# Optimization experiments

Hardware: AMD Instinct MI355X
Metric: run time of the kernel (lower is better)

## Reference

```python
import jax, jax.numpy as jnp
import numpy as np

B, C, H, W = 4, 64, 64, 64
CI = C // 4  # inter_channels for q/k convs and SE fc


def setup_inputs() -> dict:
    key = jax.random.key(0)
    ks = jax.random.split(key, 12)
    s = lambda k, shape, fan: jax.random.normal(k, shape, jnp.float32) * (1.0 / np.sqrt(fan))
    return {
        "ftr": jax.random.normal(ks[0], (B, C, H, W), jnp.float32),
        "wq": s(ks[1], (CI, C), C), "bq": jnp.zeros((CI,), jnp.float32),
        "wk": s(ks[2], (CI, C), C), "bk": jnp.zeros((CI,), jnp.float32),
        "wv": s(ks[3], (C, C), C),  "bv": jnp.zeros((C,), jnp.float32),
        "delta": jnp.array([0.1], jnp.float32),
        "w_avg1": s(ks[4], (CI, C), C), "w_avg2": s(ks[5], (C, CI), CI),
        "w_max1": s(ks[6], (CI, C), C), "w_max2": s(ks[7], (C, CI), CI),
    }


def reference(ftr, wq, bq, wk, bk, wv, bv, delta, w_avg1, w_avg2, w_max1, w_max2):
    b, c, h, w = ftr.shape
    p = h * w
    x = ftr.reshape(b, c, p)                                   # [B,C,P]
    q = jnp.einsum('oc,bcp->bpo', wq, x) + bq                  # [B,P,CI]
    k = jnp.einsum('oc,bcp->bop', wk, x) + bk[:, None]         # [B,CI,P]
    v = jnp.einsum('oc,bcp->bop', wv, x) + bv[:, None]         # [B,C,P]
    scores = jnp.einsum('bpo,boq->bpq', q, k)                  # [B,P,P]
    weights = jax.nn.softmax(scores, axis=1)                   # softmax over dim=1 (queries), as in torch code
    G = jnp.einsum('bcp,bpq->bcq', v, weights).reshape(b, c, h, w)
    out = delta[0] * G + ftr
    # ChannelRecalibration (SE with avg+max pooling)
    f_avg = jnp.mean(out, axis=(2, 3))                         # [B,C]
    f_max = jnp.max(out, axis=(2, 3))                          # [B,C]
    a = jax.nn.relu(f_avg @ w_avg1.T) @ w_avg2.T
    m = jax.nn.relu(f_max @ w_max1.T) @ w_max2.T
    gate = jax.nn.sigmoid(a + m)[:, :, None, None]
    return gate * out
```

## Files before the change

### kernel.cpp

```cpp
#include <hip/hip_runtime.h>
#include <math.h>

#define PP 4096

typedef __attribute__((ext_vector_type(8))) short short8;
typedef __attribute__((ext_vector_type(4))) float float4v;

__device__ __forceinline__ short f2bf(float f) {
    union { float f; unsigned u; } v; v.f = f;
    unsigned r = v.u + 0x7FFFu + ((v.u >> 16) & 1u);
    return (short)(r >> 16);
}

__global__ __launch_bounds__(256) void qkv_kernel(
    const float* __restrict__ ftr, const float* __restrict__ wq, const float* __restrict__ bq,
    const float* __restrict__ wk, const float* __restrict__ bk,
    const float* __restrict__ wv, const float* __restrict__ bv,
    short* __restrict__ q16, short* __restrict__ k16, short* __restrict__ v_sw)
{
    __shared__ float xs[64][68] __attribute__((aligned(16)));
    __shared__ float wvs[64][68] __attribute__((aligned(16)));
    __shared__ float wq_t[64][20] __attribute__((aligned(16)));
    __shared__ float wk_t[64][20] __attribute__((aligned(16)));

    const int b  = blockIdx.x >> 6;
    const int p0 = (blockIdx.x & 63) << 6;
    const int tid = threadIdx.x;

    for (int idx = tid; idx < 1024; idx += 256) {
        int c = idx >> 4, j4 = (idx & 15) << 2;
        *(float4*)&xs[c][j4] = *(const float4*)(ftr + ((size_t)(b * 64 + c)) * PP + p0 + j4);
    }
    for (int idx = tid; idx < 1024; idx += 256) {
        int r = idx >> 4, j4 = (idx & 15) << 2;
        *(float4*)&wvs[r][j4] = *(const float4*)(wv + r * 64 + j4);
    }
    for (int idx = tid; idx < 1024; idx += 256) {
        int o = idx >> 6, c2 = idx & 63;
        wq_t[c2][o] = wq[idx];
        wk_t[c2][o] = wk[idx];
    }
    __syncthreads();

    {
        const int wg = tid >> 6, qd = (tid >> 4) & 3, cc = tid & 15;
        const int c = wg * 16 + cc;
        const int ktg0 = p0 >> 5;
        const float bvc = bv[c];
        #pragma unroll
        for (int kt = 0; kt < 2; ++kt) {
            const int col = kt * 32 + qd * 8;
            float a[8] = {0.f,0.f,0.f,0.f,0.f,0.f,0.f,0.f};
            #pragma unroll 8
            for (int c2 = 0; c2 < 64; ++c2) {
                float w = wvs[c][c2];
                float4 xa = *(const float4*)&xs[c2][col];
                float4 xb = *(const float4*)&xs[c2][col + 4];
                a[0] += w * xa.x; a[1] += w * xa.y; a[2] += w * xa.z; a[3] += w * xa.w;
                a[4] += w * xb.x; a[5] += w * xb.y; a[6] += w * xb.z; a[7] += w * xb.w;
            }
            short8 pv;
            #pragma unroll
            for (int jj = 0; jj < 8; ++jj) pv[jj] = f2bf(a[jj] + bvc);
            *(short8*)(v_sw + ((size_t)(b * 128 + ktg0 + kt)) * 2048 + tid * 8) = pv;
        }
    }

    {
        const int p_l = tid >> 2, sel = tid & 3;
        const int half = sel & 1, arr = sel >> 1;
        const float* Wtr = arr ? &wk_t[0][0] : &wq_t[0][0];
        float a[8] = {0.f,0.f,0.f,0.f,0.f,0.f,0.f,0.f};
        #pragma unroll 8
        for (int c2 = 0; c2 < 64; ++c2) {
            float x = xs[c2][p_l];
            float4 wA = *(const float4*)(Wtr + c2 * 20 + half * 8);
            float4 wB = *(const float4*)(Wtr + c2 * 20 + half * 8 + 4);
            a[0] += wA.x * x; a[1] += wA.y * x; a[2] += wA.z * x; a[3] += wA.w * x;
            a[4] += wB.x * x; a[5] += wB.y * x; a[6] += wB.z * x; a[7] += wB.w * x;
        }
        const float* bias = arr ? bk : bq;
        const float scl = arr ? 1.0f : 1.4426950408889634f;
        short8 pq;
        #pragma unroll
        for (int oo = 0; oo < 8; ++oo)
            pq[oo] = f2bf((a[oo] + bias[half * 8 + oo]) * scl);
        short* dst = (arr ? k16 : q16) + (((size_t)(b * PP + p0 + p_l)) << 4) + half * 8;
        *(short8*)dst = pq;
    }
}

__global__ __launch_bounds__(256, 2) void attn_kernel(
    const short* __restrict__ q16, const short* __restrict__ k16,
    const short* __restrict__ v_sw,
    const float* __restrict__ ftr, const float* __restrict__ delta,
    float* __restrict__ out, float* __restrict__ psum, float* __restrict__ pmax)
{
    __shared__ char smem[34304] __attribute__((aligned(16)));
    short* Wt   = (short*)smem;
    float* Obuf = (float*)smem;
    float* lb   = (float*)(smem + 33792);

    const int b    = blockIdx.x >> 7;
    const int qblk = blockIdx.x & 127;
    const int q0   = qblk << 5;
    const int tid  = threadIdx.x;
    const int lane = tid & 63;
    const int n    = lane & 15;
    const int quad = lane >> 4;
    const int ph   = tid >> 6;

    const short8 z8 = {0,0,0,0,0,0,0,0};
    const float4v zf4 = {0.f,0.f,0.f,0.f};

    short8 bkf[2];
    #pragma unroll
    for (int mt = 0; mt < 2; ++mt) {
        bkf[mt] = z8;
        if (quad < 2)
            bkf[mt] = *(const short8*)(k16 + ((size_t)(b * PP + q0 + mt * 16 + n) << 4) + quad * 8);
    }

    const short* vbase = v_sw + (size_t)b * 262144 + lane * 8;
    const short* qbase = q16 + ((size_t)(b * PP + n) << 4) + (quad & 1) * 8;
    short* wbase = Wt + ph * 2048;

    float4v acc[2][4];
    #pragma unroll
    for (int mt = 0; mt < 2; ++mt)
        #pragma unroll
        for (int nt = 0; nt < 4; ++nt) acc[mt][nt] = zf4;
    float lsum[2] = {0.f, 0.f};

    const int pt0 = ph * 1024;
    short8 aq[2][4];
    #pragma unroll
    for (int f = 0; f < 4; ++f) { aq[0][f] = z8; aq[1][f] = z8; }
    if (quad < 2) {
        #pragma unroll
        for (int f = 0; f < 4; ++f)
            aq[0][f] = *(const short8*)(qbase + (size_t)(pt0 + f * 16) * 16);
    }

    #pragma unroll 2
    for (int it = 0; it < 16; ++it) {
        const int cb = it & 1;
        const int pt = pt0 + it * 64;
        const int ktg0 = pt >> 5;

        short8 vf[2][4];
        #pragma unroll
        for (int kt = 0; kt < 2; ++kt)
            #pragma unroll
            for (int nt = 0; nt < 4; ++nt)
                vf[kt][nt] = *(const short8*)(vbase + (size_t)((ktg0 + kt) * 4 + nt) * 512);

        if (it < 15 && quad < 2) {
            const short* qb = qbase + (size_t)(pt + 64) * 16;
            #pragma unroll
            for (int f = 0; f < 4; ++f)
                aq[cb ^ 1][f] = *(const short8*)(qb + f * 256);
        }

        float4v sf[4][2];
        #pragma unroll
        for (int f = 0; f < 4; ++f)
            #pragma unroll
            for (int mt = 0; mt < 2; ++mt)
                sf[f][mt] = __builtin_amdgcn_mfma_f32_16x16x32_bf16(aq[cb][f], bkf[mt], zf4, 0, 0, 0);

        #pragma unroll
        for (int mt = 0; mt < 2; ++mt) {
            short* wrow = wbase + (mt * 16 + n) * 64;
            #pragma unroll
            for (int f = 0; f < 4; ++f) {
                float w0 = __builtin_amdgcn_exp2f(sf[f][mt][0]);
                float w1 = __builtin_amdgcn_exp2f(sf[f][mt][1]);
                float w2 = __builtin_amdgcn_exp2f(sf[f][mt][2]);
                float w3 = __builtin_amdgcn_exp2f(sf[f][mt][3]);
                lsum[mt] += (w0 + w1) + (w2 + w3);
                uint2 pk;
                pk.x = __builtin_amdgcn_perm(__float_as_uint(w1), __float_as_uint(w0), 0x07060302u);
                pk.y = __builtin_amdgcn_perm(__float_as_uint(w3), __float_as_uint(w2), 0x07060302u);
                const int g = (f * 4 + quad) ^ ((n & 7) << 1);
                *(uint2*)(wrow + g * 4) = pk;
            }
        }

        short8 wa[2][2];
        #pragma unroll
        for (int mt = 0; mt < 2; ++mt) {
            const short* rrow = wbase + (mt * 16 + n) * 64;
            #pragma unroll
            for (int kt = 0; kt < 2; ++kt) {
                const int gr = (kt * 8 + quad * 2) ^ ((n & 7) << 1);
                wa[mt][kt] = *(const short8*)(rrow + gr * 4);
            }
        }
        #pragma unroll
        for (int mt = 0; mt < 2; ++mt)
            #pragma unroll
            for (int kt = 0; kt < 2; ++kt)
                #pragma unroll
                for (int nt = 0; nt < 4; ++nt)
                    acc[mt][nt] = __builtin_amdgcn_mfma_f32_16x16x32_bf16(wa[mt][kt], vf[kt][nt], acc[mt][nt], 0, 0, 0);
    }

    lsum[0] += __shfl_xor(lsum[0], 16); lsum[0] += __shfl_xor(lsum[0], 32);
    lsum[1] += __shfl_xor(lsum[1], 16); lsum[1] += __shfl_xor(lsum[1], 32);
    if (quad == 0) {
        lb[ph * 32 + n]      = lsum[0];
        lb[ph * 32 + 16 + n] = lsum[1];
    }
    __syncthreads();
    #pragma unroll
    for (int mt = 0; mt < 2; ++mt)
        #pragma unroll
        for (int nt = 0; nt < 4; ++nt)
            #pragma unroll
            for (int r = 0; r < 4; ++r)
                Obuf[ph * 2112 + (mt * 16 + quad * 4 + r) * 66 + nt * 16 + n] = acc[mt][nt][r];
    __syncthreads();

    const int c = tid >> 2, qq = tid & 3;
    const float dlt = delta[0];
    const size_t gbase = ((size_t)(b * 64 + c)) * PP + q0 + qq * 8;
    float4 f0 = *(const float4*)(ftr + gbase);
    float4 f1 = *(const float4*)(ftr + gbase + 4);
    float fr[8] = {f0.x, f0.y, f0.z, f0.w, f1.x, f1.y, f1.z, f1.w};
    float ov[8];
    float s8 = 0.f, m8 = -3.4e38f;
    #pragma unroll
    for (int i = 0; i < 8; ++i) {
        const int q = qq * 8 + i;
        float o = Obuf[q * 66 + c] + Obuf[2112 + q * 66 + c]
                + Obuf[4224 + q * 66 + c] + Obuf[6336 + q * 66 + c];
        float lq = lb[q] + lb[32 + q] + lb[64 + q] + lb[96 + q];
        float v = dlt * o / lq + fr[i];
        ov[i] = v; s8 += v; m8 = fmaxf(m8, v);
    }
    float4 o0 = {ov[0], ov[1], ov[2], ov[3]};
    float4 o1 = {ov[4], ov[5], ov[6], ov[7]};
    *(float4*)(out + gbase)     = o0;
    *(float4*)(out + gbase + 4) = o1;

    s8 += __shfl_xor(s8, 1); s8 += __shfl_xor(s8, 2);
    m8 = fmaxf(m8, __shfl_xor(m8, 1)); m8 = fmaxf(m8, __shfl_xor(m8, 2));
    if (qq == 0) {
        psum[((size_t)b * 128 + qblk) * 64 + c] = s8;
        pmax[((size_t)b * 128 + qblk) * 64 + c] = m8;
    }
}

__global__ __launch_bounds__(256) void reduce_gate_kernel(
    const float* __restrict__ psum, const float* __restrict__ pmax,
    const float* __restrict__ w_avg1, const float* __restrict__ w_avg2,
    const float* __restrict__ w_max1, const float* __restrict__ w_max2,
    float* __restrict__ gate)
{
    const int b = blockIdx.x, t = threadIdx.x;
    const int c = t & 63, ch = t >> 6;
    float s = 0.f, m = -3.4e38f;
    for (int i = 0; i < 32; ++i) {
        const int part = ch * 32 + i;
        s += psum[((size_t)b * 128 + part) * 64 + c];
        m = fmaxf(m, pmax[((size_t)b * 128 + part) * 64 + c]);
    }
    __shared__ float ss[4][64], sm[4][64], fa[64], fm[64], ha[16], hm[16];
    ss[ch][c] = s; sm[ch][c] = m;
    __syncthreads();
    if (t < 64) {
        fa[t] = (ss[0][t] + ss[1][t] + ss[2][t] + ss[3][t]) * (1.f / 4096.f);
        fm[t] = fmaxf(fmaxf(sm[0][t], sm[1][t]), fmaxf(sm[2][t], sm[3][t]));
    }
    __syncthreads();
    if (t < 16) {
        float a = 0.f;
        for (int cc = 0; cc < 64; ++cc) a += fa[cc] * w_avg1[t * 64 + cc];
        ha[t] = fmaxf(a, 0.f);
    } else if (t < 32) {
        float a = 0.f;
        for (int cc = 0; cc < 64; ++cc) a += fm[cc] * w_max1[(t - 16) * 64 + cc];
        hm[t - 16] = fmaxf(a, 0.f);
    }
    __syncthreads();
    if (t < 64) {
        float a = 0.f, mm = 0.f;
        #pragma unroll
        for (int i = 0; i < 16; ++i) {
            a  += ha[i] * w_avg2[t * 16 + i];
            mm += hm[i] * w_max2[t * 16 + i];
        }
        gate[b * 64 + t] = 1.f / (1.f + expf(-(a + mm)));
    }
}

__global__ __launch_bounds__(256) void mul_kernel(
    float* __restrict__ out, const float* __restrict__ gate)
{
    const float g = gate[blockIdx.x >> 2];
    const size_t e = ((size_t)blockIdx.x * 256 + threadIdx.x) * 4;
    float4 v = *(const float4*)(out + e);
    v.x *= g; v.y *= g; v.z *= g; v.w *= g;
    *(float4*)(out + e) = v;
}

extern "C" void kernel_launch(void* const* d_in, const int* in_sizes, int n_in,
                              void* d_out, int out_size, void* d_ws, size_t ws_size,
                              hipStream_t stream)
{
    const float* ftr    = (const float*)d_in[0];
    const float* wq     = (const float*)d_in[1];
    const float* bq     = (const float*)d_in[2];
    const float* wk     = (const float*)d_in[3];
    const float* bk     = (const float*)d_in[4];
    const float* wv     = (const float*)d_in[5];
    const float* bv     = (const float*)d_in[6];
    const float* delta  = (const float*)d_in[7];
    const float* w_avg1 = (const float*)d_in[8];
    const float* w_avg2 = (const float*)d_in[9];
    const float* w_max1 = (const float*)d_in[10];
    const float* w_max2 = (const float*)d_in[11];
    float* out = (float*)d_out;

    short* wsS  = (short*)d_ws;
    short* q16  = wsS;
    short* k16  = wsS + 262144;
    short* v_sw = wsS + 524288;
    float* fbase = (float*)(wsS + 1572864);
    float* psum = fbase;
    float* pmax = fbase + 32768;
    float* gate = fbase + 65536;

    qkv_kernel<<<256, 256, 0, stream>>>(ftr, wq, bq, wk, bk, wv, bv, q16, k16, v_sw);
    attn_kernel<<<512, 256, 0, stream>>>(q16, k16, v_sw, ftr, delta, out, psum, pmax);
    reduce_gate_kernel<<<4, 256, 0, stream>>>(psum, pmax, w_avg1, w_avg2, w_max1, w_max2, gate);
    mul_kernel<<<1024, 256, 0, stream>>>(out, gate);
}
```

Before: 125.0 us.

## Keep softmax weights in registers using 16x16x16 MFMA chaining, drop LDS staging

Reworks the attention kernel to use the 16x16x16 bf16 MFMA, whose output layout matches the B-operand layout. Exponentiated scores can then feed the V·W MFMA straight from registers instead of being written to and reread from shared memory. Column sums of the weights are also computed with an MFMA against a ones vector. V is stored in a new layout to match, and blocks grow to 512 threads covering 64 query columns, which halves the number of partial-sum entries. The cost is more MFMA instructions with a smaller K per instruction, higher register pressure, and a longer epilogue with several barriers.

```diff
diff --git a/kernel.cpp b/kernel.cpp
--- a/kernel.cpp
+++ b/kernel.cpp
@@ -4,6 +4,7 @@
 #define PP 4096
 
 typedef __attribute__((ext_vector_type(8))) short short8;
+typedef __attribute__((ext_vector_type(4))) short short4v;
 typedef __attribute__((ext_vector_type(4))) float float4v;
 
 __device__ __forceinline__ short f2bf(float f) {
@@ -12,11 +13,23 @@
     return (short)(r >> 16);
 }
 
+#if __has_builtin(__builtin_amdgcn_mfma_f32_16x16x16bf16_1k)
+__device__ __forceinline__ float4v mfma16(short4v a, short4v b, float4v c) {
+    return __builtin_amdgcn_mfma_f32_16x16x16bf16_1k(a, b, c, 0, 0, 0);
+}
+#else
+__device__ __forceinline__ float4v mfma16(short4v a, short4v b, float4v c) {
+    short8 a8 = {a[0], a[1], a[2], a[3], 0, 0, 0, 0};
+    short8 b8 = {b[0], b[1], b[2], b[3], 0, 0, 0, 0};
+    return __builtin_amdgcn_mfma_f32_16x16x32_bf16(a8, b8, c, 0, 0, 0);
+}
+#endif
+
 __global__ __launch_bounds__(256) void qkv_kernel(
     const float* __restrict__ ftr, const float* __restrict__ wq, const float* __restrict__ bq,
     const float* __restrict__ wk, const float* __restrict__ bk,
     const float* __restrict__ wv, const float* __restrict__ bv,
-    short* __restrict__ q16, short* __restrict__ k16, short* __restrict__ v_sw)
+    short* __restrict__ q16, short* __restrict__ k16, short* __restrict__ v_a)
 {
     __shared__ float xs[64][68] __attribute__((aligned(16)));
     __shared__ float wvs[64][68] __attribute__((aligned(16)));
@@ -45,7 +58,6 @@
     {
         const int wg = tid >> 6, qd = (tid >> 4) & 3, cc = tid & 15;
         const int c = wg * 16 + cc;
-        const int ktg0 = p0 >> 5;
         const float bvc = bv[c];
         #pragma unroll
         for (int kt = 0; kt < 2; ++kt) {
@@ -59,10 +71,15 @@
                 a[0] += w * xa.x; a[1] += w * xa.y; a[2] += w * xa.z; a[3] += w * xa.w;
                 a[4] += w * xb.x; a[5] += w * xb.y; a[6] += w * xb.z; a[7] += w * xb.w;
             }
-            short8 pv;
-            #pragma unroll
-            for (int jj = 0; jj < 8; ++jj) pv[jj] = f2bf(a[jj] + bvc);
-            *(short8*)(v_sw + ((size_t)(b * 128 + ktg0 + kt)) * 2048 + tid * 8) = pv;
+            const int ptg = ((p0 + kt * 32) >> 4) + (qd >> 1);
+            const int qp0 = (qd & 1) * 2;
+            #pragma unroll
+            for (int h = 0; h < 2; ++h) {
+                short4v pv;
+                #pragma unroll
+                for (int j = 0; j < 4; ++j) pv[j] = f2bf(a[h * 4 + j] + bvc);
+                *(short4v*)(v_a + ((((size_t)(b * 256 + ptg)) * 4 + wg) * 64 + (qp0 + h) * 16 + cc) * 4) = pv;
+            }
         }
     }
 
@@ -90,165 +107,145 @@
     }
 }
 
-__global__ __launch_bounds__(256, 2) void attn_kernel(
+__global__ __launch_bounds__(512, 2) void attn_kernel(
     const short* __restrict__ q16, const short* __restrict__ k16,
-    const short* __restrict__ v_sw,
+    const short* __restrict__ v_a,
     const float* __restrict__ ftr, const float* __restrict__ delta,
     float* __restrict__ out, float* __restrict__ psum, float* __restrict__ pmax)
 {
-    __shared__ char smem[34304] __attribute__((aligned(16)));
-    short* Wt   = (short*)smem;
-    float* Obuf = (float*)smem;
-    float* lb   = (float*)(smem + 33792);
-
-    const int b    = blockIdx.x >> 7;
-    const int qblk = blockIdx.x & 127;
-    const int q0   = qblk << 5;
+    __shared__ float Obuf[8][16][66];
+    __shared__ float lb[8][64];
+    __shared__ float lfin[64];
+
+    const int b    = blockIdx.x >> 6;
+    const int qblk = blockIdx.x & 63;
+    const int q0   = qblk << 6;
     const int tid  = threadIdx.x;
     const int lane = tid & 63;
     const int n    = lane & 15;
     const int quad = lane >> 4;
     const int ph   = tid >> 6;
 
-    const short8 z8 = {0,0,0,0,0,0,0,0};
-    const float4v zf4 = {0.f,0.f,0.f,0.f};
-
-    short8 bkf[2];
+    const float4v zf4 = {0.f, 0.f, 0.f, 0.f};
+    const short4v ones = {0x3F80, 0x3F80, 0x3F80, 0x3F80};
+
+    short4v bkf[4];
     #pragma unroll
-    for (int mt = 0; mt < 2; ++mt) {
-        bkf[mt] = z8;
-        if (quad < 2)
-            bkf[mt] = *(const short8*)(k16 + ((size_t)(b * PP + q0 + mt * 16 + n) << 4) + quad * 8);
-    }
-
-    const short* vbase = v_sw + (size_t)b * 262144 + lane * 8;
-    const short* qbase = q16 + ((size_t)(b * PP + n) << 4) + (quad & 1) * 8;
-    short* wbase = Wt + ph * 2048;
-
-    float4v acc[2][4];
+    for (int nt = 0; nt < 4; ++nt)
+        bkf[nt] = *(const short4v*)(k16 + ((size_t)(b * PP + q0 + nt * 16 + n) << 4) + quad * 4);
+
+    const short* qrow = q16 + ((size_t)(b * PP + n) << 4) + quad * 4;
+    const short* vrow = v_a + (size_t)b * 262144 + lane * 4;
+
+    float4v acc[4][4], lacc[4];
     #pragma unroll
-    for (int mt = 0; mt < 2; ++mt)
+    for (int mt = 0; mt < 4; ++mt)
         #pragma unroll
         for (int nt = 0; nt < 4; ++nt) acc[mt][nt] = zf4;
-    float lsum[2] = {0.f, 0.f};
-
-    const int pt0 = ph * 1024;
-    short8 aq[2][4];
     #pragma unroll
-    for (int f = 0; f < 4; ++f) { aq[0][f] = z8; aq[1][f] = z8; }
-    if (quad < 2) {
+    for (int nt = 0; nt < 4; ++nt) lacc[nt] = zf4;
+
+    const int pt0 = ph * 512;
+    for (int it = 0; it < 8; ++it) {
+        const int pt = pt0 + it * 64;
+        const int pti = pt >> 4;
+
+        short4v aq[4];
         #pragma unroll
         for (int f = 0; f < 4; ++f)
-            aq[0][f] = *(const short8*)(qbase + (size_t)(pt0 + f * 16) * 16);
-    }
-
-    #pragma unroll 2
-    for (int it = 0; it < 16; ++it) {
-        const int cb = it & 1;
-        const int pt = pt0 + it * 64;
-        const int ktg0 = pt >> 5;
-
-        short8 vf[2][4];
-        #pragma unroll
-        for (int kt = 0; kt < 2; ++kt)
-            #pragma unroll
-            for (int nt = 0; nt < 4; ++nt)
-                vf[kt][nt] = *(const short8*)(vbase + (size_t)((ktg0 + kt) * 4 + nt) * 512);
-
-        if (it < 15 && quad < 2) {
-            const short* qb = qbase + (size_t)(pt + 64) * 16;
-            #pragma unroll
-            for (int f = 0; f < 4; ++f)
-                aq[cb ^ 1][f] = *(const short8*)(qb + f * 256);
-        }
-
-        float4v sf[4][2];
+            aq[f] = *(const short4v*)(qrow + (size_t)(pt + f * 16) * 16);
+        short4v va[4][4];
         #pragma unroll
         for (int f = 0; f < 4; ++f)
             #pragma unroll
-            for (int mt = 0; mt < 2; ++mt)
-                sf[f][mt] = __builtin_amdgcn_mfma_f32_16x16x32_bf16(aq[cb][f], bkf[mt], zf4, 0, 0, 0);
-
-        #pragma unroll
-        for (int mt = 0; mt < 2; ++mt) {
-            short* wrow = wbase + (mt * 16 + n) * 64;
-            #pragma unroll
-            for (int f = 0; f < 4; ++f) {
-                float w0 = __builtin_amdgcn_exp2f(sf[f][mt][0]);
-                float w1 = __builtin_amdgcn_exp2f(sf[f][mt][1]);
-                float w2 = __builtin_amdgcn_exp2f(sf[f][mt][2]);
-                float w3 = __builtin_amdgcn_exp2f(sf[f][mt][3]);
-                lsum[mt] += (w0 + w1) + (w2 + w3);
-                uint2 pk;
-                pk.x = __builtin_amdgcn_perm(__float_as_uint(w1), __float_as_uint(w0), 0x07060302u);
-                pk.y = __builtin_amdgcn_perm(__float_as_uint(w3), __float_as_uint(w2), 0x07060302u);
-                const int g = (f * 4 + quad) ^ ((n & 7) << 1);
-                *(uint2*)(wrow + g * 4) = pk;
-            }
-        }
-
-        short8 wa[2][2];
-        #pragma unroll
-        for (int mt = 0; mt < 2; ++mt) {
-            const short* rrow = wbase + (mt * 16 + n) * 64;
-            #pragma unroll
-            for (int kt = 0; kt < 2; ++kt) {
-                const int gr = (kt * 8 + quad * 2) ^ ((n & 7) << 1);
-                wa[mt][kt] = *(const short8*)(rrow + gr * 4);
-            }
-        }
-        #pragma unroll
-        for (int mt = 0; mt < 2; ++mt)
-            #pragma unroll
-            for (int kt = 0; kt < 2; ++kt)
+            for (int mt = 0; mt < 4; ++mt)
+                va[f][mt] = *(const short4v*)(vrow + (size_t)((pti + f) * 4 + mt) * 256);
+
+        float4v sf_c[4], sf_n[4];
+        #pragma unroll
+        for (int nt = 0; nt < 4; ++nt)
+            sf_c[nt] = mfma16(aq[0], bkf[nt], zf4);
+
+        #pragma unroll
+        for (int f = 0; f < 4; ++f) {
+            if (f < 3) {
                 #pragma unroll
                 for (int nt = 0; nt < 4; ++nt)
-                    acc[mt][nt] = __builtin_amdgcn_mfma_f32_16x16x32_bf16(wa[mt][kt], vf[kt][nt], acc[mt][nt], 0, 0, 0);
-    }
-
-    lsum[0] += __shfl_xor(lsum[0], 16); lsum[0] += __shfl_xor(lsum[0], 32);
-    lsum[1] += __shfl_xor(lsum[1], 16); lsum[1] += __shfl_xor(lsum[1], 32);
+                    sf_n[nt] = mfma16(aq[f + 1], bkf[nt], zf4);
+            }
+            short4v w[4];
+            #pragma unroll
+            for (int nt = 0; nt < 4; ++nt) {
+                float w0 = __builtin_amdgcn_exp2f(sf_c[nt][0]);
+                float w1 = __builtin_amdgcn_exp2f(sf_c[nt][1]);
+                float w2 = __builtin_amdgcn_exp2f(sf_c[nt][2]);
+                float w3 = __builtin_amdgcn_exp2f(sf_c[nt][3]);
+                union { uint2 u; short4v s; } cv;
+                cv.u.x = __builtin_amdgcn_perm(__float_as_uint(w1), __float_as_uint(w0), 0x07060302u);
+                cv.u.y = __builtin_amdgcn_perm(__float_as_uint(w3), __float_as_uint(w2), 0x07060302u);
+                w[nt] = cv.s;
+            }
+            #pragma unroll
+            for (int nt = 0; nt < 4; ++nt)
+                lacc[nt] = mfma16(ones, w[nt], lacc[nt]);
+            #pragma unroll
+            for (int mt = 0; mt < 4; ++mt)
+                #pragma unroll
+                for (int nt = 0; nt < 4; ++nt)
+                    acc[mt][nt] = mfma16(va[f][mt], w[nt], acc[mt][nt]);
+            #pragma unroll
+            for (int nt = 0; nt < 4; ++nt) sf_c[nt] = sf_n[nt];
+        }
+    }
+
     if (quad == 0) {
-        lb[ph * 32 + n]      = lsum[0];
-        lb[ph * 32 + 16 + n] = lsum[1];
-    }
-    __syncthreads();
+        #pragma unroll
+        for (int nt = 0; nt < 4; ++nt)
+            lb[ph][nt * 16 + n] = lacc[nt][0];
+    }
+    __syncthreads();
+    if (tid < 64) {
+        float s = 0.f;
+        #pragma unroll
+        for (int p8 = 0; p8 < 8; ++p8) s += lb[p8][tid];
+        lfin[tid] = delta[0] / s;
+    }
+    __syncthreads();
+
+    const int c_l = tid >> 5;
+    const int q2  = (tid & 31) * 2;
     #pragma unroll
-    for (int mt = 0; mt < 2; ++mt)
+    for (int mt = 0; mt < 4; ++mt) {
         #pragma unroll
         for (int nt = 0; nt < 4; ++nt)
             #pragma unroll
-            for (int r = 0; r < 4; ++r)
-                Obuf[ph * 2112 + (mt * 16 + quad * 4 + r) * 66 + nt * 16 + n] = acc[mt][nt][r];
-    __syncthreads();
-
-    const int c = tid >> 2, qq = tid & 3;
-    const float dlt = delta[0];
-    const size_t gbase = ((size_t)(b * 64 + c)) * PP + q0 + qq * 8;
-    float4 f0 = *(const float4*)(ftr + gbase);
-    float4 f1 = *(const float4*)(ftr + gbase + 4);
-    float fr[8] = {f0.x, f0.y, f0.z, f0.w, f1.x, f1.y, f1.z, f1.w};
-    float ov[8];
-    float s8 = 0.f, m8 = -3.4e38f;
-    #pragma unroll
-    for (int i = 0; i < 8; ++i) {
-        const int q = qq * 8 + i;
-        float o = Obuf[q * 66 + c] + Obuf[2112 + q * 66 + c]
-                + Obuf[4224 + q * 66 + c] + Obuf[6336 + q * 66 + c];
-        float lq = lb[q] + lb[32 + q] + lb[64 + q] + lb[96 + q];
-        float v = dlt * o / lq + fr[i];
-        ov[i] = v; s8 += v; m8 = fmaxf(m8, v);
-    }
-    float4 o0 = {ov[0], ov[1], ov[2], ov[3]};
-    float4 o1 = {ov[4], ov[5], ov[6], ov[7]};
-    *(float4*)(out + gbase)     = o0;
-    *(float4*)(out + gbase + 4) = o1;
-
-    s8 += __shfl_xor(s8, 1); s8 += __shfl_xor(s8, 2);
-    m8 = fmaxf(m8, __shfl_xor(m8, 1)); m8 = fmaxf(m8, __shfl_xor(m8, 2));
-    if (qq == 0) {
-        psum[((size_t)b * 128 + qblk) * 64 + c] = s8;
-        pmax[((size_t)b * 128 + qblk) * 64 + c] = m8;
+            for (int i = 0; i < 4; ++i)
+                Obuf[ph][quad * 4 + i][nt * 16 + n] = acc[mt][nt][i];
+        __syncthreads();
+        const int c = mt * 16 + c_l;
+        float o0 = 0.f, o1 = 0.f;
+        #pragma unroll
+        for (int p8 = 0; p8 < 8; ++p8) {
+            o0 += Obuf[p8][c_l][q2];
+            o1 += Obuf[p8][c_l][q2 + 1];
+        }
+        const size_t g = ((size_t)(b * 64 + c)) * PP + q0 + q2;
+        float2 fv = *(const float2*)(ftr + g);
+        o0 = o0 * lfin[q2]     + fv.x;
+        o1 = o1 * lfin[q2 + 1] + fv.y;
+        float2 ov; ov.x = o0; ov.y = o1;
+        *(float2*)(out + g) = ov;
+        float s = o0 + o1, m = fmaxf(o0, o1);
+        s += __shfl_xor(s, 1); s += __shfl_xor(s, 2);
+        s += __shfl_xor(s, 4); s += __shfl_xor(s, 8); s += __shfl_xor(s, 16);
+        m = fmaxf(m, __shfl_xor(m, 1)); m = fmaxf(m, __shfl_xor(m, 2));
+        m = fmaxf(m, __shfl_xor(m, 4)); m = fmaxf(m, __shfl_xor(m, 8));
+        m = fmaxf(m, __shfl_xor(m, 16));
+        if ((tid & 31) == 0) {
+            psum[((size_t)(b * 64) + qblk) * 64 + c] = s;
+            pmax[((size_t)(b * 64) + qblk) * 64 + c] = m;
+        }
+        __syncthreads();
     }
 }
 
@@ -261,10 +258,10 @@
     const int b = blockIdx.x, t = threadIdx.x;
     const int c = t & 63, ch = t >> 6;
     float s = 0.f, m = -3.4e38f;
-    for (int i = 0; i < 32; ++i) {
-        const int part = ch * 32 + i;
-        s += psum[((size_t)b * 128 + part) * 64 + c];
-        m = fmaxf(m, pmax[((size_t)b * 128 + part) * 64 + c]);
+    for (int i = 0; i < 16; ++i) {
+        const int qb = ch * 16 + i;
+        s += psum[((size_t)(b * 64) + qb) * 64 + c];
+        m = fmaxf(m, pmax[((size_t)(b * 64) + qb) * 64 + c]);
     }
     __shared__ float ss[4][64], sm[4][64], fa[64], fm[64], ha[16], hm[16];
     ss[ch][c] = s; sm[ch][c] = m;
@@ -326,14 +323,14 @@
     short* wsS  = (short*)d_ws;
     short* q16  = wsS;
     short* k16  = wsS + 262144;
-    short* v_sw = wsS + 524288;
+    short* v_a  = wsS + 524288;
     float* fbase = (float*)(wsS + 1572864);
     float* psum = fbase;
-    float* pmax = fbase + 32768;
-    float* gate = fbase + 65536;
-
-    qkv_kernel<<<256, 256, 0, stream>>>(ftr, wq, bq, wk, bk, wv, bv, q16, k16, v_sw);
-    attn_kernel<<<512, 256, 0, stream>>>(q16, k16, v_sw, ftr, delta, out, psum, pmax);
+    float* pmax = fbase + 16384;
+    float* gate = fbase + 32768;
+
+    qkv_kernel<<<256, 256, 0, stream>>>(ftr, wq, bq, wk, bk, wv, bv, q16, k16, v_a);
+    attn_kernel<<<256, 512, 0, stream>>>(q16, k16, v_a, ftr, delta, out, psum, pmax);
     reduce_gate_kernel<<<4, 256, 0, stream>>>(psum, pmax, w_avg1, w_avg2, w_max1, w_max2, gate);
     mul_kernel<<<1024, 256, 0, stream>>>(out, gate);
 }
```

Result: slower. 129.0 us (+3.1%).
